# Kernel tuning notes

Measured on AMD Instinct MI355X. Metric: run time of the kernel, lower is better.

The kernel has to match this reference:

```python
import jax, jax.numpy as jnp
import numpy as np

N_HEADS = 16

def setup_inputs() -> dict:
    key = jax.random.key(0)
    k1, k2 = jax.random.split(key)
    B, S, H = 4, 2048, 1024
    hidden_states = jax.random.normal(k1, (B, S, H), dtype=jnp.float32)
    # F.linear weight: [out_features, in_features]; init std per module
    std = 0.02 / np.sqrt(2.0 * 24 * H)
    queries_weight = jax.random.normal(k2, (H, H), dtype=jnp.float32) * std
    return {"hidden_states": hidden_states, "queries_weight": queries_weight}


def reference(hidden_states, queries_weight):
    B, S, H = hidden_states.shape
    hd = H // N_HEADS
    # F.linear: x @ W^T
    q = hidden_states @ queries_weight.T
    qh = q.reshape(B, S, N_HEADS, hd)          # [B,S,h,d]
    xh = hidden_states.reshape(B, S, N_HEADS, hd)
    # pre_attn = Q K^T (no softmax), then attn @ V with K=V=x heads
    pre_attn = jnp.einsum('bqhd,bkhd->bhqk', qh, xh)   # [B,h,S,S]
    attn = jnp.einsum('bhqk,bkhd->bqhd', pre_attn, xh) # [B,S,h,d]
    return attn.reshape(B, S, H)
```

## Files before the change

kernel.cpp:

```cpp
#include <hip/hip_runtime.h>
#include <hip/hip_bf16.h>


typedef __bf16 bf16x8 __attribute__((ext_vector_type(8)));
typedef float f32x4 __attribute__((ext_vector_type(4)));

typedef __attribute__((address_space(3))) unsigned int lds_u32;
typedef const __attribute__((address_space(1))) unsigned int glb_u32;

__device__ __forceinline__ void gld_lds16(const void* g, void* l) {
    __builtin_amdgcn_global_load_lds((glb_u32*)g, (lds_u32*)l, 16, 0, 0);
}

__device__ __forceinline__ unsigned short f2bf(float f) {
    unsigned int u = __float_as_uint(f);
    u += 0x7FFFu + ((u >> 16) & 1u);
    return (unsigned short)(u >> 16);
}

__global__ __launch_bounds__(256) void gx_partial(
        const float* __restrict__ x, const float* __restrict__ W,
        unsigned short* __restrict__ xb, unsigned short* __restrict__ Wb,
        float* __restrict__ Gp) {
    __shared__ __align__(16) unsigned short xt[2][64 * 128];
    const int tid = threadIdx.x;
    const int chunk = blockIdx.x;
    const int bh = blockIdx.y;
    const int fb = bh * 8 + chunk;
    const int b = bh >> 4, h = bh & 15;
    const int wave = tid >> 6, lane = tid & 63;
    const int lm = lane & 15, quad = lane >> 4;

    {
        size_t base = (size_t)fb * 2048 + (size_t)tid * 8;
        float4 v0 = *(const float4*)&W[base];
        float4 v1 = *(const float4*)&W[base + 4];
        ushort4 o0 = {f2bf(v0.x), f2bf(v0.y), f2bf(v0.z), f2bf(v0.w)};
        ushort4 o1 = {f2bf(v1.x), f2bf(v1.y), f2bf(v1.z), f2bf(v1.w)};
        *(ushort4*)&Wb[base] = o0;
        *(ushort4*)&Wb[base + 4] = o1;
    }

    const int sc = (tid & 15) * 4;
    const int sr = tid >> 4;
    const size_t gcol = (size_t)h * 64 + sc;
    const int wsz0 = ((tid & 7) ^ 0) << 3;
    const int wsz1 = ((tid & 7) ^ 2) << 3;
    const int wsz2 = ((tid & 7) ^ 4) << 3;
    const int wsz3 = ((tid & 7) ^ 6) << 3;
    const int rA = wave * 16 + lm;
    const int swzA = ((((rA >> 2) & 7) ^ ((rA & 3) << 1)) << 3);
    int swzB[4];
    #pragma unroll
    for (int ni = 0; ni < 4; ++ni) {
        int rb = ni * 16 + lm;
        swzB[ni] = ((((rb >> 2) & 7) ^ ((rb & 3) << 1)) << 3);
    }
    const int colq = quad * 8;
    const size_t row0 = (size_t)(b * 2048 + chunk * 256);

    f32x4 acc[4] = {};
    float4 v[8];

    #pragma unroll
    for (int i = 0; i < 8; ++i)
        v[i] = *(const float4*)&x[(row0 + sr + 16 * i) * 1024 + gcol];
    #pragma unroll
    for (int i = 0; i < 8; ++i) {
        int s = sr + 16 * i;
        ushort4 o = {f2bf(v[i].x), f2bf(v[i].y), f2bf(v[i].z), f2bf(v[i].w)};
        *(ushort4*)&xb[(row0 + s) * 1024 + gcol] = o;
        xt[0][(sc + 0) * 128 + (s ^ wsz0)] = o.x;
        xt[0][(sc + 1) * 128 + (s ^ wsz1)] = o.y;
        xt[0][(sc + 2) * 128 + (s ^ wsz2)] = o.z;
        xt[0][(sc + 3) * 128 + (s ^ wsz3)] = o.w;
    }
    __syncthreads();

    #pragma unroll
    for (int i = 0; i < 8; ++i)
        v[i] = *(const float4*)&x[(row0 + 128 + sr + 16 * i) * 1024 + gcol];

    #pragma unroll
    for (int k = 0; k < 4; ++k) {
        bf16x8 af = *(const bf16x8*)&xt[0][rA * 128 + ((k * 32 + colq) ^ swzA)];
        #pragma unroll
        for (int ni = 0; ni < 4; ++ni) {
            bf16x8 bg = *(const bf16x8*)&xt[0][(ni * 16 + lm) * 128 + ((k * 32 + colq) ^ swzB[ni])];
            acc[ni] = __builtin_amdgcn_mfma_f32_16x16x32_bf16(af, bg, acc[ni], 0, 0, 0);
        }
    }

    #pragma unroll
    for (int i = 0; i < 8; ++i) {
        int s = sr + 16 * i;
        ushort4 o = {f2bf(v[i].x), f2bf(v[i].y), f2bf(v[i].z), f2bf(v[i].w)};
        *(ushort4*)&xb[(row0 + 128 + s) * 1024 + gcol] = o;
        xt[1][(sc + 0) * 128 + (s ^ wsz0)] = o.x;
        xt[1][(sc + 1) * 128 + (s ^ wsz1)] = o.y;
        xt[1][(sc + 2) * 128 + (s ^ wsz2)] = o.z;
        xt[1][(sc + 3) * 128 + (s ^ wsz3)] = o.w;
    }
    __syncthreads();

    #pragma unroll
    for (int k = 0; k < 4; ++k) {
        bf16x8 af = *(const bf16x8*)&xt[1][rA * 128 + ((k * 32 + colq) ^ swzA)];
        #pragma unroll
        for (int ni = 0; ni < 4; ++ni) {
            bf16x8 bg = *(const bf16x8*)&xt[1][(ni * 16 + lm) * 128 + ((k * 32 + colq) ^ swzB[ni])];
            acc[ni] = __builtin_amdgcn_mfma_f32_16x16x32_bf16(af, bg, acc[ni], 0, 0, 0);
        }
    }

    float* gp = Gp + ((size_t)(chunk * 64 + bh)) * 4096;
    #pragma unroll
    for (int ni = 0; ni < 4; ++ni)
        #pragma unroll
        for (int r = 0; r < 4; ++r)
            gp[(wave * 16 + quad * 4 + r) * 64 + ni * 16 + lm] = acc[ni][r];
}

__global__ __launch_bounds__(256) void g_reduce(
        const float* __restrict__ Gp, unsigned short* __restrict__ Gb) {
    const int bh = blockIdx.x;
    const int e0 = blockIdx.y * 1024 + threadIdx.x * 4;
    float4 s = {0.f, 0.f, 0.f, 0.f};
    #pragma unroll
    for (int c = 0; c < 8; ++c) {
        float4 v = *(const float4*)&Gp[((size_t)(c * 64 + bh)) * 4096 + e0];
        s.x += v.x; s.y += v.y; s.z += v.z; s.w += v.w;
    }
    ushort4 o;
    o.x = f2bf(s.x); o.y = f2bf(s.y); o.z = f2bf(s.z); o.w = f2bf(s.w);
    *(ushort4*)&Gb[(size_t)bh * 4096 + e0] = o;
}

__global__ __launch_bounds__(512, 1) void gemm_qout(
        const unsigned short* __restrict__ xb, const unsigned short* __restrict__ Wb,
        const unsigned short* __restrict__ Gb, float* __restrict__ out) {
    extern __shared__ __align__(16) unsigned short smem[];
    const int tid = threadIdx.x;
    const int m0 = blockIdx.x * 256;
    const int n0 = blockIdx.y * 128;
    const int b  = blockIdx.x >> 3;
    const int h0 = blockIdx.y * 2;
    const int lane = tid & 63, wave = tid >> 6;
    const int wr = (wave >> 1) * 64;
    const int wc = (wave & 1) * 64;
    const int lm = lane & 15, quad = lane >> 4;
    const int srow8 = lane >> 3;
    const int scol = (((lane & 7) ^ (srow8 & 7))) * 8;

    const unsigned short* gaBase = &xb[(size_t)(m0 + wave * 32 + srow8) * 1024 + scol];
    const unsigned short* gbBase = &Wb[(size_t)(n0 + wave * 16 + srow8) * 1024 + scol];

    unsigned short* A0 = smem;
    unsigned short* B0 = smem + 16384;
    unsigned short* A1 = smem + 24576;
    unsigned short* B1 = smem + 40960;
    unsigned short* A2 = smem + 49152;
    unsigned short* B2 = smem + 65536;

#define STAGE(pA, pB, KT)                                                     \
    {                                                                         \
        _Pragma("unroll")                                                     \
        for (int i = 0; i < 4; ++i)                                           \
            gld_lds16(gaBase + (KT) + (size_t)i * 8 * 1024,                   \
                      &(pA)[(wave * 32 + i * 8) * 64]);                       \
        _Pragma("unroll")                                                     \
        for (int i = 0; i < 2; ++i)                                           \
            gld_lds16(gbBase + (KT) + (size_t)i * 8 * 1024,                   \
                      &(pB)[(wave * 16 + i * 8) * 64]);                       \
    }

#define COMPUTE(pA, pB)                                                       \
    {                                                                         \
        _Pragma("unroll")                                                     \
        for (int kk = 0; kk < 2; ++kk) {                                      \
            bf16x8 af[4], bg[4];                                              \
            _Pragma("unroll")                                                 \
            for (int mi = 0; mi < 4; ++mi) {                                  \
                int ra = wr + mi * 16 + lm;                                   \
                int jb = (kk * 4 + quad) ^ (ra & 7);                          \
                af[mi] = *(const bf16x8*)&(pA)[ra * 64 + jb * 8];             \
            }                                                                 \
            _Pragma("unroll")                                                 \
            for (int ni = 0; ni < 4; ++ni) {                                  \
                int rb = wc + ni * 16 + lm;                                   \
                int jb = (kk * 4 + quad) ^ (rb & 7);                          \
                bg[ni] = *(const bf16x8*)&(pB)[rb * 64 + jb * 8];             \
            }                                                                 \
            _Pragma("unroll")                                                 \
            for (int mi = 0; mi < 4; ++mi)                                    \
                _Pragma("unroll")                                             \
                for (int ni = 0; ni < 4; ++ni)                                \
                    acc[mi][ni] = __builtin_amdgcn_mfma_f32_16x16x32_bf16(    \
                        af[mi], bg[ni], acc[mi][ni], 0, 0, 0);                \
        }                                                                     \
    }

    f32x4 acc[4][4] = {};
    STAGE(A0, B0, 0);
    STAGE(A1, B1, 64);
    for (int t = 0; t < 16; ++t) {
        if (t < 14) {
            STAGE(A2, B2, (t + 2) * 64);
            asm volatile("s_waitcnt vmcnt(12)" ::: "memory");
        } else if (t == 14) {
            asm volatile("s_waitcnt vmcnt(6)" ::: "memory");
        } else {
            asm volatile("s_waitcnt vmcnt(0)" ::: "memory");
        }
        __builtin_amdgcn_sched_barrier(0);
        asm volatile("s_barrier" ::: "memory");
        __builtin_amdgcn_s_setprio(1);
        COMPUTE(A0, B0);
        __builtin_amdgcn_s_setprio(0);
        asm volatile("s_barrier" ::: "memory");
        unsigned short* tA = A0; A0 = A1; A1 = A2; A2 = tA;
        unsigned short* tB = B0; B0 = B1; B1 = B2; B2 = tB;
    }
#undef STAGE
#undef COMPUTE

    unsigned short* Qt = smem;
    unsigned short* G2 = smem + 34816;
    #pragma unroll
    for (int mi = 0; mi < 4; ++mi)
        #pragma unroll
        for (int ni = 0; ni < 4; ++ni)
            #pragma unroll
            for (int r = 0; r < 4; ++r)
                Qt[(wr + mi * 16 + quad * 4 + r) * 136 + wc + ni * 16 + lm] =
                    f2bf(acc[mi][ni][r]);
    #pragma unroll
    for (int i = 0; i < 2; ++i) {
        int idx = tid + 512 * i;
        int hh = idx >> 9;
        int rr = (idx >> 3) & 63;
        int cc = (idx & 7) * 8;
        *(uint4*)&G2[hh * 4608 + rr * 72 + cc] =
            *(const uint4*)&Gb[((size_t)(b * 16 + h0 + hh)) * 4096 + rr * 64 + cc];
    }
    asm volatile("s_barrier" ::: "memory");
    #pragma unroll
    for (int mi = 0; mi < 4; ++mi)
        #pragma unroll
        for (int ni = 0; ni < 4; ++ni)
            acc[mi][ni] = (f32x4){0.f, 0.f, 0.f, 0.f};
    const int hh = wave & 1;
    #pragma unroll
    for (int kk = 0; kk < 2; ++kk) {
        bf16x8 af[4], bg[4];
        #pragma unroll
        for (int mi = 0; mi < 4; ++mi)
            af[mi] = *(const bf16x8*)&Qt[(wr + mi * 16 + lm) * 136 + wc + kk * 32 + quad * 8];
        #pragma unroll
        for (int ni = 0; ni < 4; ++ni)
            bg[ni] = *(const bf16x8*)&G2[hh * 4608 + (ni * 16 + lm) * 72 + kk * 32 + quad * 8];
        #pragma unroll
        for (int mi = 0; mi < 4; ++mi)
            #pragma unroll
            for (int ni = 0; ni < 4; ++ni)
                acc[mi][ni] = __builtin_amdgcn_mfma_f32_16x16x32_bf16(
                    af[mi], bg[ni], acc[mi][ni], 0, 0, 0);
    }
    #pragma unroll
    for (int mi = 0; mi < 4; ++mi)
        #pragma unroll
        for (int ni = 0; ni < 4; ++ni)
            #pragma unroll
            for (int r = 0; r < 4; ++r)
                out[(size_t)(m0 + wr + mi * 16 + quad * 4 + r) * 1024
                    + n0 + wc + ni * 16 + lm] = acc[mi][ni][r];
}

extern "C" void kernel_launch(void* const* d_in, const int* in_sizes, int n_in,
                              void* d_out, int out_size, void* d_ws, size_t ws_size,
                              hipStream_t stream) {
    const float* x = (const float*)d_in[0];
    const float* W = (const float*)d_in[1];
    float* out = (float*)d_out;
    char* ws = (char*)d_ws;
    unsigned short* xb = (unsigned short*)(ws);
    unsigned short* Wb = (unsigned short*)(ws + 16777216);
    float*          Gp = (float*)        (ws + 18874368);
    unsigned short* Gb = (unsigned short*)(ws + 27262976);

    gx_partial<<<dim3(8, 64), 256, 0, stream>>>(x, W, xb, Wb, Gp);
    g_reduce<<<dim3(64, 4), 256, 0, stream>>>(Gp, Gb);
    gemm_qout<<<dim3(32, 8), 512, 147456, stream>>>(xb, Wb, Gb, out);
}
```

Before: 114.9 us.

## Restructure Q-out GEMM to 256 threads, BK=32, two blocks per CU

The Q-projection GEMM now runs with 4 waves of 256 threads instead of 8. Each wave computes a 128x64 tile with 8x4 MFMA accumulators, and the K tile shrinks from 64 to 32 so the triple-buffered LDS fits in 72KB of static shared memory. The goal is two resident blocks per CU for better latency hiding, with a new XOR swizzle for 32-wide rows. The epilogue gives each wave a private Qt region and reads G directly from global memory rather than staging it in LDS, which removes a block barrier. The cost is doubled accumulator register pressure, twice as many K-loop iterations and barriers, and uncoalesced global reads of G.

After: 117.9 us. 2.6% more time.

```diff
diff --git a/kernel.cpp b/kernel.cpp
--- a/kernel.cpp
+++ b/kernel.cpp
@@ -136,78 +136,68 @@
     *(ushort4*)&Gb[(size_t)bh * 4096 + e0] = o;
 }
 
-__global__ __launch_bounds__(512, 1) void gemm_qout(
+__global__ __launch_bounds__(256, 2) void gemm_qout(
         const unsigned short* __restrict__ xb, const unsigned short* __restrict__ Wb,
         const unsigned short* __restrict__ Gb, float* __restrict__ out) {
-    extern __shared__ __align__(16) unsigned short smem[];
+    __shared__ __align__(16) unsigned short smem[36864];
     const int tid = threadIdx.x;
     const int m0 = blockIdx.x * 256;
     const int n0 = blockIdx.y * 128;
     const int b  = blockIdx.x >> 3;
     const int h0 = blockIdx.y * 2;
     const int lane = tid & 63, wave = tid >> 6;
-    const int wr = (wave >> 1) * 64;
+    const int wr = (wave >> 1) * 128;
     const int wc = (wave & 1) * 64;
     const int lm = lane & 15, quad = lane >> 4;
-    const int srow8 = lane >> 3;
-    const int scol = (((lane & 7) ^ (srow8 & 7))) * 8;
-
-    const unsigned short* gaBase = &xb[(size_t)(m0 + wave * 32 + srow8) * 1024 + scol];
-    const unsigned short* gbBase = &Wb[(size_t)(n0 + wave * 16 + srow8) * 1024 + scol];
-
-    unsigned short* A0 = smem;
-    unsigned short* B0 = smem + 16384;
-    unsigned short* A1 = smem + 24576;
-    unsigned short* B1 = smem + 40960;
-    unsigned short* A2 = smem + 49152;
-    unsigned short* B2 = smem + 65536;
-
-#define STAGE(pA, pB, KT)                                                     \
+    const int sr16 = lane >> 2;
+    const int sg = (sr16 ^ (sr16 >> 2)) & 3;
+    const int scol = ((lane & 3) ^ sg) * 8;
+    const int jb8 = (quad ^ ((lm ^ (lm >> 2)) & 3)) * 8;
+
+    const unsigned short* gaB = &xb[(size_t)(m0 + wave * 64 + sr16) * 1024 + scol];
+    const unsigned short* gbB = &Wb[(size_t)(n0 + wave * 32 + sr16) * 1024 + scol];
+
+    unsigned short* buf0 = smem;
+    unsigned short* buf1 = smem + 12288;
+    unsigned short* buf2 = smem + 24576;
+
+#define STAGE(pB, KT)                                                         \
     {                                                                         \
         _Pragma("unroll")                                                     \
         for (int i = 0; i < 4; ++i)                                           \
-            gld_lds16(gaBase + (KT) + (size_t)i * 8 * 1024,                   \
-                      &(pA)[(wave * 32 + i * 8) * 64]);                       \
+            gld_lds16(gaB + (KT) + (size_t)i * 16 * 1024,                     \
+                      &(pB)[(wave * 64 + i * 16) * 32]);                      \
         _Pragma("unroll")                                                     \
         for (int i = 0; i < 2; ++i)                                           \
-            gld_lds16(gbBase + (KT) + (size_t)i * 8 * 1024,                   \
-                      &(pB)[(wave * 16 + i * 8) * 64]);                       \
-    }
-
-#define COMPUTE(pA, pB)                                                       \
+            gld_lds16(gbB + (KT) + (size_t)i * 16 * 1024,                     \
+                      &(pB)[8192 + (wave * 32 + i * 16) * 32]);               \
+    }
+
+#define COMPUTE(pB)                                                           \
     {                                                                         \
-        _Pragma("unroll")                                                     \
-        for (int kk = 0; kk < 2; ++kk) {                                      \
-            bf16x8 af[4], bg[4];                                              \
+        bf16x8 af[8], bg[4];                                                  \
+        _Pragma("unroll")                                                     \
+        for (int mi = 0; mi < 8; ++mi)                                        \
+            af[mi] = *(const bf16x8*)&(pB)[(wr + mi * 16 + lm) * 32 + jb8];   \
+        _Pragma("unroll")                                                     \
+        for (int ni = 0; ni < 4; ++ni)                                        \
+            bg[ni] = *(const bf16x8*)&(pB)[8192 + (wc + ni * 16 + lm) * 32 + jb8]; \
+        _Pragma("unroll")                                                     \
+        for (int mi = 0; mi < 8; ++mi)                                        \
             _Pragma("unroll")                                                 \
-            for (int mi = 0; mi < 4; ++mi) {                                  \
-                int ra = wr + mi * 16 + lm;                                   \
-                int jb = (kk * 4 + quad) ^ (ra & 7);                          \
-                af[mi] = *(const bf16x8*)&(pA)[ra * 64 + jb * 8];             \
-            }                                                                 \
-            _Pragma("unroll")                                                 \
-            for (int ni = 0; ni < 4; ++ni) {                                  \
-                int rb = wc + ni * 16 + lm;                                   \
-                int jb = (kk * 4 + quad) ^ (rb & 7);                          \
-                bg[ni] = *(const bf16x8*)&(pB)[rb * 64 + jb * 8];             \
-            }                                                                 \
-            _Pragma("unroll")                                                 \
-            for (int mi = 0; mi < 4; ++mi)                                    \
-                _Pragma("unroll")                                             \
-                for (int ni = 0; ni < 4; ++ni)                                \
-                    acc[mi][ni] = __builtin_amdgcn_mfma_f32_16x16x32_bf16(    \
-                        af[mi], bg[ni], acc[mi][ni], 0, 0, 0);                \
-        }                                                                     \
-    }
-
-    f32x4 acc[4][4] = {};
-    STAGE(A0, B0, 0);
-    STAGE(A1, B1, 64);
-    for (int t = 0; t < 16; ++t) {
-        if (t < 14) {
-            STAGE(A2, B2, (t + 2) * 64);
+            for (int ni = 0; ni < 4; ++ni)                                    \
+                acc[mi][ni] = __builtin_amdgcn_mfma_f32_16x16x32_bf16(        \
+                    af[mi], bg[ni], acc[mi][ni], 0, 0, 0);                    \
+    }
+
+    f32x4 acc[8][4] = {};
+    STAGE(buf0, 0);
+    STAGE(buf1, 32);
+    for (int t = 0; t < 32; ++t) {
+        if (t < 30) {
+            STAGE(buf2, (t + 2) * 32);
             asm volatile("s_waitcnt vmcnt(12)" ::: "memory");
-        } else if (t == 14) {
+        } else if (t == 30) {
             asm volatile("s_waitcnt vmcnt(6)" ::: "memory");
         } else {
             asm volatile("s_waitcnt vmcnt(0)" ::: "memory");
@@ -215,59 +205,48 @@
         __builtin_amdgcn_sched_barrier(0);
         asm volatile("s_barrier" ::: "memory");
         __builtin_amdgcn_s_setprio(1);
-        COMPUTE(A0, B0);
+        COMPUTE(buf0);
         __builtin_amdgcn_s_setprio(0);
         asm volatile("s_barrier" ::: "memory");
-        unsigned short* tA = A0; A0 = A1; A1 = A2; A2 = tA;
-        unsigned short* tB = B0; B0 = B1; B1 = B2; B2 = tB;
+        unsigned short* tp = buf0; buf0 = buf1; buf1 = buf2; buf2 = tp;
     }
 #undef STAGE
 #undef COMPUTE
 
-    unsigned short* Qt = smem;
-    unsigned short* G2 = smem + 34816;
-    #pragma unroll
-    for (int mi = 0; mi < 4; ++mi)
+    unsigned short* Qt = smem + wave * 9216;
+    #pragma unroll
+    for (int mi = 0; mi < 8; ++mi)
         #pragma unroll
         for (int ni = 0; ni < 4; ++ni)
             #pragma unroll
             for (int r = 0; r < 4; ++r)
-                Qt[(wr + mi * 16 + quad * 4 + r) * 136 + wc + ni * 16 + lm] =
+                Qt[(mi * 16 + quad * 4 + r) * 72 + ni * 16 + lm] =
                     f2bf(acc[mi][ni][r]);
     #pragma unroll
-    for (int i = 0; i < 2; ++i) {
-        int idx = tid + 512 * i;
-        int hh = idx >> 9;
-        int rr = (idx >> 3) & 63;
-        int cc = (idx & 7) * 8;
-        *(uint4*)&G2[hh * 4608 + rr * 72 + cc] =
-            *(const uint4*)&Gb[((size_t)(b * 16 + h0 + hh)) * 4096 + rr * 64 + cc];
-    }
-    asm volatile("s_barrier" ::: "memory");
-    #pragma unroll
-    for (int mi = 0; mi < 4; ++mi)
+    for (int mi = 0; mi < 8; ++mi)
         #pragma unroll
         for (int ni = 0; ni < 4; ++ni)
             acc[mi][ni] = (f32x4){0.f, 0.f, 0.f, 0.f};
     const int hh = wave & 1;
+    const unsigned short* gsrc = &Gb[((size_t)(b * 16 + h0 + hh)) * 4096];
     #pragma unroll
     for (int kk = 0; kk < 2; ++kk) {
-        bf16x8 af[4], bg[4];
-        #pragma unroll
-        for (int mi = 0; mi < 4; ++mi)
-            af[mi] = *(const bf16x8*)&Qt[(wr + mi * 16 + lm) * 136 + wc + kk * 32 + quad * 8];
-        #pragma unroll
-        for (int ni = 0; ni < 4; ++ni)
-            bg[ni] = *(const bf16x8*)&G2[hh * 4608 + (ni * 16 + lm) * 72 + kk * 32 + quad * 8];
-        #pragma unroll
-        for (int mi = 0; mi < 4; ++mi)
+        bf16x8 af[8], bg[4];
+        #pragma unroll
+        for (int mi = 0; mi < 8; ++mi)
+            af[mi] = *(const bf16x8*)&Qt[(mi * 16 + lm) * 72 + kk * 32 + quad * 8];
+        #pragma unroll
+        for (int ni = 0; ni < 4; ++ni)
+            bg[ni] = *(const bf16x8*)&gsrc[(ni * 16 + lm) * 64 + kk * 32 + quad * 8];
+        #pragma unroll
+        for (int mi = 0; mi < 8; ++mi)
             #pragma unroll
             for (int ni = 0; ni < 4; ++ni)
                 acc[mi][ni] = __builtin_amdgcn_mfma_f32_16x16x32_bf16(
                     af[mi], bg[ni], acc[mi][ni], 0, 0, 0);
     }
     #pragma unroll
-    for (int mi = 0; mi < 4; ++mi)
+    for (int mi = 0; mi < 8; ++mi)
         #pragma unroll
         for (int ni = 0; ni < 4; ++ni)
             #pragma unroll
@@ -290,5 +269,5 @@
 
     gx_partial<<<dim3(8, 64), 256, 0, stream>>>(x, W, xb, Wb, Gp);
     g_reduce<<<dim3(64, 4), 256, 0, stream>>>(Gp, Gb);
-    gemm_qout<<<dim3(32, 8), 512, 147456, stream>>>(xb, Wb, Gb, out);
-}
+    gemm_qout<<<dim3(32, 8), 256, 0, stream>>>(xb, Wb, Gb, out);
+}
```
